# Kernel tuning notes

Measured on AMD Instinct MI355X. Metric: run time of the kernel, lower is better.

Reference implementation:

```python
import jax, jax.numpy as jnp
import numpy as np

N = 100000   # nodes
E = 3200000  # edges
F_IN = 64    # input feature dim
H = 64       # hidden dim
G = 512      # graphs in batch
C = 6        # classes
BN_EPS = 1e-5


def setup_inputs() -> dict:
    key = jax.random.key(0)
    ks = jax.random.split(key, 24)

    def nrm(i, shape, s=0.05):
        return jax.random.normal(ks[i], shape, jnp.float32) * s

    d = {}
    d["x"] = jax.random.normal(ks[0], (N, F_IN), jnp.float32)
    d["edge_index"] = jax.random.randint(ks[1], (2, E), 0, N, dtype=jnp.int32)
    d["batch"] = jnp.sort(jax.random.randint(ks[2], (N,), 0, G, dtype=jnp.int32))
    # GIN MLP weights (conv4 reuses conv3's MLP, matching the original code)
    for li, fin in [(1, F_IN), (2, H), (3, H)]:
        d[f"w{li}a"] = nrm(2 + li * 4, (fin, H))
        d[f"b{li}a"] = jnp.zeros((H,), jnp.float32)
        d[f"w{li}b"] = nrm(3 + li * 4, (H, H))
        d[f"b{li}b"] = jnp.zeros((H,), jnp.float32)
    # learnable eps (train_eps=True, init 0) and BN affine params per layer
    for li in range(1, 5):
        d[f"eps{li}"] = jnp.float32(0.0)
        d[f"g{li}"] = jnp.ones((H,), jnp.float32)
        d[f"be{li}"] = jnp.zeros((H,), jnp.float32)
    d["wfc"] = nrm(20, (2 * H, C))
    d["bfc"] = jnp.zeros((C,), jnp.float32)
    return d


def gin_block(x, src, dst, eps, wa, ba, wb, bb, gamma, beta):
    # neighbor sum aggregation: messages flow src -> dst
    agg = jax.ops.segment_sum(x[src], dst, num_segments=N)
    h = (1.0 + eps) * x + agg
    h = jax.nn.relu(h @ wa + ba) @ wb + bb  # GIN MLP
    h = jax.nn.relu(h)
    # BatchNorm1d over the node dimension (training-mode batch stats)
    mu = h.mean(axis=0)
    var = h.var(axis=0)
    return (h - mu) * jax.lax.rsqrt(var + BN_EPS) * gamma + beta


def reference(x, edge_index, batch,
              w1a, b1a, w1b, b1b, w2a, b2a, w2b, b2b, w3a, b3a, w3b, b3b,
              eps1, g1, be1, eps2, g2, be2, eps3, g3, be3, eps4, g4, be4,
              wfc, bfc):
    src, dst = edge_index[0], edge_index[1]
    h = gin_block(x, src, dst, eps1, w1a, b1a, w1b, b1b, g1, be1)
    h = gin_block(h, src, dst, eps2, w2a, b2a, w2b, b2b, g2, be2)
    h = gin_block(h, src, dst, eps3, w3a, b3a, w3b, b3b, g3, be3)
    # conv4 shares nn3's weights (faithful to the original source)
    h = gin_block(h, src, dst, eps4, w3a, b3a, w3b, b3b, g4, be4)
    cnt = jax.ops.segment_sum(jnp.ones((N, 1), h.dtype), batch, num_segments=G)
    meanp = jax.ops.segment_sum(h, batch, num_segments=G) / jnp.maximum(cnt, 1.0)
    maxp = jax.ops.segment_max(h, batch, num_segments=G)
    maxp = jnp.where(cnt > 0, maxp, 0.0)
    pooled = jnp.concatenate([meanp, maxp], axis=1)  # [G, 128]
    return jax.nn.log_softmax(pooled @ wfc + bfc, axis=1)
```

## Files before the change

### kernel.cpp

```cpp
#include <hip/hip_runtime.h>

#define N_NODES 100000
#define N_EDGES 3200000
#define NGRAPH 512
#define NCLASS 6
#define BN_EPS 1e-5f

#define BSHIFT 8
#define NBUCK 391
#define CHUNK 8192
#define EB 391
#define NBLK_NODE 391
#define FUSG 3125
#define NPART 6250
#define CAST_B 6250
#define BSMAX 12032

typedef unsigned short u16;
typedef unsigned int u32;
typedef __attribute__((ext_vector_type(8))) short bf16x8;
typedef __attribute__((ext_vector_type(4))) float f32x4;
typedef __attribute__((ext_vector_type(2))) float f32x2;

__device__ __forceinline__ float bflo(u32 b) {
    u32 t = b << 16; return __builtin_bit_cast(float, t);
}
__device__ __forceinline__ float bfhi(u32 b) {
    u32 t = b & 0xffff0000u; return __builtin_bit_cast(float, t);
}
__device__ __forceinline__ f32x2 bfpair(u32 b) {
    return (f32x2){bflo(b), bfhi(b)};
}
__device__ __forceinline__ u16 f2bf(float f) {
    u32 u = __builtin_bit_cast(u32, f);
    return (u16)((u + 0x7fffu + ((u >> 16) & 1u)) >> 16);
}

__global__ void k_setup(const float* __restrict__ x, u16* __restrict__ xb,
                        const float* __restrict__ W10, const float* __restrict__ W20,
                        const float* __restrict__ W11, const float* __restrict__ W21,
                        const float* __restrict__ W12, const float* __restrict__ W22,
                        u16* __restrict__ Wtg, float* __restrict__ ss0,
                        const int* __restrict__ dst, const int* __restrict__ batch,
                        int* __restrict__ blockhist, int* __restrict__ gstart,
                        int* __restrict__ rowstart) {
    __shared__ int hist[NBUCK];
    int b = blockIdx.x;
    int t = threadIdx.x;
    if (b < CAST_B) {
        int base = (b * 256 + t) * 4;
        float4 v = *(const float4*)(x + base);
        ushort4 o = make_ushort4(f2bf(v.x), f2bf(v.y), f2bf(v.z), f2bf(v.w));
        *(ushort4*)(xb + base) = o;
    } else if (b < CAST_B + 97) {
        int bb = b - CAST_B;
        if (bb < 96) {
            int e = bb * 256 + t;
            int mat = e >> 12;
            int i = e & 4095;
            const float* s = (mat == 0) ? W10 : (mat == 1) ? W20 : (mat == 2) ? W11
                           : (mat == 3) ? W21 : (mat == 4) ? W12 : W22;
            float v = s[i];
            int k = i >> 6, c = i & 63;
            Wtg[mat * 4608 + c * 72 + k] = f2bf(v);
        } else {
            if (t < 64) ss0[t] = 1.0f;
            else if (t < 128) ss0[t] = 0.0f;
            else if (t == 128) rowstart[N_NODES] = N_EDGES;
        }
    } else if (b < CAST_B + 97 + EB) {
        int be = b - (CAST_B + 97);
        long e0 = (long)be * CHUNK;
        for (int i = t; i < NBUCK; i += 256) hist[i] = 0;
        __syncthreads();
        for (int i = t; i < CHUNK; i += 256) {
            long e = e0 + i;
            if (e < N_EDGES) atomicAdd(&hist[dst[e] >> BSHIFT], 1);
        }
        __syncthreads();
        for (int i = t; i < NBUCK; i += 256) blockhist[be * NBUCK + i] = hist[i];
    } else {
        int i = (b - (CAST_B + 97 + EB)) * 256 + t;
        if (i < N_NODES) {
            int bi = batch[i];
            int bp = (i == 0) ? -1 : batch[i - 1];
            for (int g = bp + 1; g <= bi; ++g) gstart[g] = i;
            if (i == N_NODES - 1)
                for (int g = bi + 1; g <= NGRAPH; ++g) gstart[g] = N_NODES;
        }
    }
}

__global__ void k_scan_cols(int* __restrict__ blockhist, int* __restrict__ colsum) {
    __shared__ int sh[512];
    int k = blockIdx.x;
    int t = threadIdx.x;
    int v = (t < EB) ? blockhist[t * NBUCK + k] : 0;
    sh[t] = v;
    __syncthreads();
    for (int off = 1; off < 512; off <<= 1) {
        int x = (t >= off) ? sh[t - off] : 0;
        __syncthreads();
        sh[t] += x;
        __syncthreads();
    }
    if (t < EB) blockhist[t * NBUCK + k] = sh[t] - v;
    if (t == 511) colsum[k] = sh[511];
}

__global__ __launch_bounds__(512) void k_bscatter(
    const int* __restrict__ src, const int* __restrict__ dst,
    const int* __restrict__ colsum, const int* __restrict__ blockhist,
    int* __restrict__ pairs) {
    __shared__ int sh[512];
    __shared__ int bstart_s[NBUCK];
    __shared__ int cnt[NBUCK];
    __shared__ int cur[NBUCK];
    __shared__ int gbase[NBUCK];
    __shared__ u32 sorted[CHUNK];
    __shared__ u16 kbuf[CHUNK];
    int t = threadIdx.x;
    int b = blockIdx.x;
    long e0 = (long)b * CHUNK;
    int v = (t < NBUCK) ? colsum[t] : 0;
    sh[t] = v;
    if (t < NBUCK) cnt[t] = 0;
    __syncthreads();
    for (int off = 1; off < 512; off <<= 1) {
        int x = (t >= off) ? sh[t - off] : 0;
        __syncthreads();
        sh[t] += x;
        __syncthreads();
    }
    if (t < NBUCK) bstart_s[t] = sh[t] - v;
    __syncthreads();
    for (int i = t; i < CHUNK; i += 512) {
        long e = e0 + i;
        if (e < N_EDGES) atomicAdd(&cnt[dst[e] >> BSHIFT], 1);
    }
    __syncthreads();
    int c = (t < NBUCK) ? cnt[t] : 0;
    sh[t] = c;
    __syncthreads();
    for (int off = 1; off < 512; off <<= 1) {
        int x = (t >= off) ? sh[t - off] : 0;
        __syncthreads();
        sh[t] += x;
        __syncthreads();
    }
    if (t < NBUCK) {
        int excl = sh[t] - c;
        cur[t] = excl;
        gbase[t] = bstart_s[t] + blockhist[b * NBUCK + t] - excl;
    }
    __syncthreads();
    for (int i = t; i < CHUNK; i += 512) {
        long e = e0 + i;
        if (e < N_EDGES) {
            int d = dst[e];
            int k = d >> BSHIFT;
            int r = atomicAdd(&cur[k], 1);
            sorted[r] = ((u32)src[e] << 8) | (u32)(d & 255);
            kbuf[r] = (u16)k;
        }
    }
    __syncthreads();
    int tot = (int)min((long)CHUNK, (long)N_EDGES - e0);
    for (int i = t; i < tot; i += 512)
        pairs[gbase[kbuf[i]] + i] = (int)sorted[i];
}

__global__ __launch_bounds__(512) void k_bsort(
    const int* __restrict__ pairs, const int* __restrict__ colsum,
    int* __restrict__ rowstart, int* __restrict__ esrc) {
    __shared__ int sh[512];
    __shared__ int deg[256];
    __shared__ int cur[256];
    __shared__ u32 ssrc[BSMAX];
    int b = blockIdx.x;
    int t = threadIdx.x;
    int v = (t < NBUCK) ? colsum[t] : 0;
    sh[t] = v;
    if (t < 256) deg[t] = 0;
    __syncthreads();
    for (int off = 1; off < 512; off <<= 1) {
        int x = (t >= off) ? sh[t - off] : 0;
        __syncthreads();
        sh[t] += x;
        __syncthreads();
    }
    int p0 = (b == 0) ? 0 : sh[b - 1];
    int p1 = sh[b];
    int n = p1 - p0;
    __syncthreads();
    for (int i = p0 + t; i < p1; i += 512)
        atomicAdd(&deg[pairs[i] & 255], 1);
    __syncthreads();
    if (t < 256) sh[t] = deg[t];
    __syncthreads();
    for (int off = 1; off < 256; off <<= 1) {
        int x = (t >= off && t < 256) ? sh[t - off] : 0;
        __syncthreads();
        if (t < 256) sh[t] += x;
        __syncthreads();
    }
    if (t < 256) {
        int excl = sh[t] - deg[t];
        cur[t] = excl;
        int node = (b << BSHIFT) + t;
        if (node < N_NODES) rowstart[node] = p0 + excl;
    }
    __syncthreads();
    if (n <= BSMAX) {
        for (int i = p0 + t; i < p1; i += 512) {
            u32 pr = (u32)pairs[i];
            int r = atomicAdd(&cur[pr & 255], 1);
            ssrc[r] = pr >> 8;
        }
        __syncthreads();
        for (int i = t; i < n; i += 512) esrc[p0 + i] = (int)ssrc[i];
    } else {
        for (int i = p0 + t; i < p1; i += 512) {
            u32 pr = (u32)pairs[i];
            int r = atomicAdd(&cur[pr & 255], 1);
            esrc[p0 + r] = (int)(pr >> 8);
        }
    }
}

__global__ void k_bn(const float* __restrict__ partials, const float* __restrict__ g,
                     const float* __restrict__ be, float* __restrict__ ss) {
    __shared__ float sS[256];
    __shared__ float sQ[256];
    int f = blockIdx.x;
    int t = threadIdx.x;
    float aS = 0.f, aQ = 0.f;
    for (int b = t; b < NPART; b += 256) {
        aS += partials[b * 128 + f];
        aQ += partials[b * 128 + 64 + f];
    }
    sS[t] = aS; sQ[t] = aQ;
    __syncthreads();
    for (int off = 128; off >= 1; off >>= 1) {
        if (t < off) { sS[t] += sS[t + off]; sQ[t] += sQ[t + off]; }
        __syncthreads();
    }
    if (t == 0) {
        float mu = sS[0] / (float)N_NODES;
        float var = fmaxf(sQ[0] / (float)N_NODES - mu * mu, 0.f);
        float sc = g[f] * rsqrtf(var + BN_EPS);
        ss[f] = sc;
        ss[64 + f] = be[f] - mu * sc;
    }
}

__global__ __launch_bounds__(128, 5) void k_fused(
    const u16* __restrict__ hin, const float* __restrict__ ss,
    const float* __restrict__ epsp, const int* __restrict__ rowstart,
    const int* __restrict__ esrc, const u16* __restrict__ Wt,
    const float* __restrict__ b1, const float* __restrict__ b2,
    u16* __restrict__ C, float* __restrict__ partials) {
    __shared__ __align__(16) u16 Ain[2][16 * 72];
    __shared__ __align__(16) u16 Hs[2][16 * 72];
    int lane = threadIdx.x & 63;
    int wid = threadIdx.x >> 6;
    int r0 = blockIdx.x * 32 + wid * 16;

    int g = lane >> 3;
    int p = lane & 7;
    int f0 = 8 * p;

    float epsv = 1.0f + epsp[0];
    float4 scA = *(const float4*)(ss + f0);
    float4 scB = *(const float4*)(ss + f0 + 4);
    float4 shA = *(const float4*)(ss + 64 + f0);
    float4 shB = *(const float4*)(ss + 64 + f0 + 4);
    float sc[8] = {scA.x, scA.y, scA.z, scA.w, scB.x, scB.y, scB.z, scB.w};
    float sh[8] = {shA.x, shA.y, shA.z, shA.w, shB.x, shB.y, shB.z, shB.w};

    int rs = rowstart[r0 + ((lane < 17) ? lane : 16)];

    #pragma unroll
    for (int half = 0; half < 2; ++half) {
        int t = g + 8 * half;
        int node = r0 + t;
        int e0 = __shfl(rs, t);
        int e1 = __shfl(rs, t + 1);
        uint4 sb = *(const uint4*)(hin + (unsigned)node * 64u + f0);
        f32x2 aA0 = {0.f, 0.f}, aA1 = {0.f, 0.f}, aA2 = {0.f, 0.f}, aA3 = {0.f, 0.f};
        f32x2 aB0 = {0.f, 0.f}, aB1 = {0.f, 0.f}, aB2 = {0.f, 0.f}, aB3 = {0.f, 0.f};
        int e = e0;
        int e_full = e0 + ((e1 - e0) & ~7);
        for (; e < e_full; e += 8) {
            #pragma unroll
            for (int k = 0; k < 8; ++k) {
                int a = esrc[e + k];
                uint4 v = *(const uint4*)(hin + (unsigned)a * 64u + f0);
                if (k & 1) {
                    aB0 += bfpair(v.x); aB1 += bfpair(v.y);
                    aB2 += bfpair(v.z); aB3 += bfpair(v.w);
                } else {
                    aA0 += bfpair(v.x); aA1 += bfpair(v.y);
                    aA2 += bfpair(v.z); aA3 += bfpair(v.w);
                }
            }
        }
        for (; e < e1; ++e) {
            int a = esrc[e];
            uint4 v = *(const uint4*)(hin + (unsigned)a * 64u + f0);
            aA0 += bfpair(v.x); aA1 += bfpair(v.y);
            aA2 += bfpair(v.z); aA3 += bfpair(v.w);
        }
        f32x2 ac0 = aA0 + aB0, ac1 = aA1 + aB1, ac2 = aA2 + aB2, ac3 = aA3 + aB3;
        float acc[8] = {ac0.x, ac0.y, ac1.x, ac1.y, ac2.x, ac2.y, ac3.x, ac3.y};
        float self[8] = {bflo(sb.x), bfhi(sb.x), bflo(sb.y), bfhi(sb.y),
                         bflo(sb.z), bfhi(sb.z), bflo(sb.w), bfhi(sb.w)};
        float deg = (float)(e1 - e0);
        u32 pk[4];
        #pragma unroll
        for (int k = 0; k < 4; ++k) {
            float oa = sc[2 * k] * (acc[2 * k] + epsv * self[2 * k]) +
                       (deg + epsv) * sh[2 * k];
            float ob = sc[2 * k + 1] * (acc[2 * k + 1] + epsv * self[2 * k + 1]) +
                       (deg + epsv) * sh[2 * k + 1];
            pk[k] = (u32)f2bf(oa) | ((u32)f2bf(ob) << 16);
        }
        u32* arow = (u32*)&Ain[wid][0] + t * 36 + p * 4;
        *(uint4*)arow = make_uint4(pk[0], pk[1], pk[2], pk[3]);
    }

    const u16* Wt2 = Wt + 4608;
    int m = lane & 15;
    int q = lane >> 4;

    bf16x8 a0 = *(const bf16x8*)(&Ain[wid][m * 72 + q * 8]);
    bf16x8 a1 = *(const bf16x8*)(&Ain[wid][m * 72 + 32 + q * 8]);
    f32x4 acc[4];
    #pragma unroll
    for (int c = 0; c < 4; ++c) {
        acc[c] = (f32x4){0.f, 0.f, 0.f, 0.f};
        bf16x8 bA = *(const bf16x8*)(Wt + (c * 16 + m) * 72 + q * 8);
        bf16x8 bB = *(const bf16x8*)(Wt + (c * 16 + m) * 72 + 32 + q * 8);
        acc[c] = __builtin_amdgcn_mfma_f32_16x16x32_bf16(a0, bA, acc[c], 0, 0, 0);
        acc[c] = __builtin_amdgcn_mfma_f32_16x16x32_bf16(a1, bB, acc[c], 0, 0, 0);
    }
    #pragma unroll
    for (int c = 0; c < 4; ++c) {
        int col = c * 16 + m;
        float bb = b1[col];
        #pragma unroll
        for (int r = 0; r < 4; ++r)
            Hs[wid][(q * 4 + r) * 72 + col] = f2bf(fmaxf(acc[c][r] + bb, 0.f));
    }
    bf16x8 h0 = *(const bf16x8*)(&Hs[wid][m * 72 + q * 8]);
    bf16x8 h1 = *(const bf16x8*)(&Hs[wid][m * 72 + 32 + q * 8]);
    f32x4 acc2[4];
    #pragma unroll
    for (int c = 0; c < 4; ++c) {
        acc2[c] = (f32x4){0.f, 0.f, 0.f, 0.f};
        bf16x8 bA = *(const bf16x8*)(Wt2 + (c * 16 + m) * 72 + q * 8);
        bf16x8 bB = *(const bf16x8*)(Wt2 + (c * 16 + m) * 72 + 32 + q * 8);
        acc2[c] = __builtin_amdgcn_mfma_f32_16x16x32_bf16(h0, bA, acc2[c], 0, 0, 0);
        acc2[c] = __builtin_amdgcn_mfma_f32_16x16x32_bf16(h1, bB, acc2[c], 0, 0, 0);
    }
    size_t prow = ((size_t)blockIdx.x * 2 + wid) * 128;
    #pragma unroll
    for (int c = 0; c < 4; ++c) {
        int col = c * 16 + m;
        float bb = b2[col];
        float psum = 0.f, psq = 0.f;
        #pragma unroll
        for (int r = 0; r < 4; ++r) {
            int rg = r0 + q * 4 + r;
            float o = fmaxf(acc2[c][r] + bb, 0.f);
            C[(size_t)rg * 64 + col] = f2bf(o);
            psum += o;
            psq += o * o;
        }
        psum += __shfl_xor(psum, 16);
        psum += __shfl_xor(psum, 32);
        psq += __shfl_xor(psq, 16);
        psq += __shfl_xor(psq, 32);
        if (q == 0) {
            partials[prow + col] = psum;
            partials[prow + 64 + col] = psq;
        }
    }
}

__global__ void k_pool(const u16* __restrict__ h, const float* __restrict__ ss,
                       const int* __restrict__ gstart, const float* __restrict__ wfc,
                       const float* __restrict__ bfc, float* __restrict__ out) {
    __shared__ float smean[2][128];
    __shared__ float smax[2][128];
    __shared__ float lg[2][8];
    int tid = threadIdx.x;
    int lane = tid & 63;
    int w = tid >> 6;
    int gi = w >> 1;
    int part = w & 1;
    int gr = blockIdx.x * 2 + gi;
    int half = lane >> 5;
    int li = lane & 31;
    int f0 = 2 * li;
    float sc0 = ss[f0], sc1 = ss[f0 + 1];
    float sh0 = ss[64 + f0], sh1 = ss[64 + f0 + 1];
    int s0n = gstart[gr], s1n = gstart[gr + 1];
    int cnt = s1n - s0n;
    int mid = s0n + (cnt >> 1);
    int a = part ? mid : s0n;
    int b = part ? s1n : mid;
    float sum0 = 0.f, sum1 = 0.f, mx0 = -3.4e38f, mx1 = -3.4e38f;
    for (int n = a + half; n < b; n += 2) {
        u32 bits = *(const u32*)(h + (size_t)n * 64 + f0);
        float x0 = fmaf(bflo(bits), sc0, sh0);
        float x1 = fmaf(bfhi(bits), sc1, sh1);
        sum0 += x0; sum1 += x1;
        mx0 = fmaxf(mx0, x0); mx1 = fmaxf(mx1, x1);
    }
    sum0 += __shfl_xor(sum0, 32);
    sum1 += __shfl_xor(sum1, 32);
    mx0 = fmaxf(mx0, __shfl_xor(mx0, 32));
    mx1 = fmaxf(mx1, __shfl_xor(mx1, 32));
    if (half == 0 && part == 0) {
        smean[gi][f0] = sum0; smean[gi][f0 + 1] = sum1;
        smax[gi][f0] = mx0;   smax[gi][f0 + 1] = mx1;
    }
    __syncthreads();
    if (half == 0 && part == 1) {
        float m0 = fmaxf(smax[gi][f0], mx0), m1 = fmaxf(smax[gi][f0 + 1], mx1);
        float t0 = smean[gi][f0] + sum0, t1 = smean[gi][f0 + 1] + sum1;
        float fc = fmaxf((float)cnt, 1.f);
        smean[gi][f0] = t0 / fc;
        smean[gi][f0 + 1] = t1 / fc;
        smax[gi][f0] = (cnt > 0) ? m0 : 0.f;
        smax[gi][f0 + 1] = (cnt > 0) ? m1 : 0.f;
    }
    __syncthreads();
    if (part == 0 && lane < NCLASS) {
        float acc = bfc[lane];
        for (int j = 0; j < 64; ++j) acc = fmaf(smean[gi][j], wfc[j * NCLASS + lane], acc);
        for (int j = 0; j < 64; ++j) acc = fmaf(smax[gi][j], wfc[(64 + j) * NCLASS + lane], acc);
        lg[gi][lane] = acc;
    }
    __syncthreads();
    if (part == 0 && lane < NCLASS) {
        float mm = -3.4e38f;
        for (int c = 0; c < NCLASS; ++c) mm = fmaxf(mm, lg[gi][c]);
        float se = 0.f;
        for (int c = 0; c < NCLASS; ++c) se += expf(lg[gi][c] - mm);
        out[gr * NCLASS + lane] = lg[gi][lane] - mm - logf(se);
    }
}


extern "C" void kernel_launch(void* const* d_in, const int* in_sizes, int n_in,
                              void* d_out, int out_size, void* d_ws, size_t ws_size,
                              hipStream_t stream) {
    const float* x = (const float*)d_in[0];
    const int* ei = (const int*)d_in[1];
    const int* batch = (const int*)d_in[2];
    const int* esrc_in = ei;
    const int* edst_in = ei + N_EDGES;

    const float* ba[4] = {(const float*)d_in[4], (const float*)d_in[8],
                          (const float*)d_in[12], (const float*)d_in[12]};
    const float* bb[4] = {(const float*)d_in[6], (const float*)d_in[10],
                          (const float*)d_in[14], (const float*)d_in[14]};
    const float* epsv[4] = {(const float*)d_in[15], (const float*)d_in[18],
                            (const float*)d_in[21], (const float*)d_in[24]};
    const float* gg[4] = {(const float*)d_in[16], (const float*)d_in[19],
                          (const float*)d_in[22], (const float*)d_in[25]};
    const float* bee[4] = {(const float*)d_in[17], (const float*)d_in[20],
                           (const float*)d_in[23], (const float*)d_in[26]};
    const float* wfc = (const float*)d_in[27];
    const float* bfc = (const float*)d_in[28];
    float* out = (float*)d_out;

    char* ws = (char*)d_ws;
    int* pairs = (int*)(ws + 0);
    u16* bufA = (u16*)(ws + 0);
    int* esrc = (int*)(ws + 12800000);
    u16* xb = (u16*)(ws + 25600000);
    u16* bufB = (u16*)(ws + 38400000);
    int* rowstart = (int*)(ws + 51200000);
    int* blockhist = (int*)(ws + 51600128);
    int* colsum = (int*)(ws + 52212480);
    int* gstart = (int*)(ws + 52214528);
    float* partials = (float*)(ws + 52217088);
    float* ssbuf = (float*)(ws + 55417600);
    u16* Wtg = (u16*)(ws + 55420160);

    k_setup<<<CAST_B + 97 + EB + NBLK_NODE, 256, 0, stream>>>(
        x, xb, (const float*)d_in[3], (const float*)d_in[5], (const float*)d_in[7],
        (const float*)d_in[9], (const float*)d_in[11], (const float*)d_in[13],
        Wtg, ssbuf, edst_in, batch, blockhist, gstart, rowstart);
    k_scan_cols<<<NBUCK, 512, 0, stream>>>(blockhist, colsum);
    k_bscatter<<<EB, 512, 0, stream>>>(esrc_in, edst_in, colsum, blockhist, pairs);
    k_bsort<<<NBUCK, 512, 0, stream>>>(pairs, colsum, rowstart, esrc);

    const u16* hb[4] = {xb, bufB, bufA, bufB};
    u16* cb[4] = {bufB, bufA, bufB, bufA};
    for (int L = 0; L < 4; ++L) {
        const u16* wt = Wtg + (size_t)((L < 2) ? L : 2) * 9216;
        k_fused<<<FUSG, 128, 0, stream>>>(hb[L], ssbuf + L * 128, epsv[L], rowstart,
                                          esrc, wt, ba[L], bb[L], cb[L], partials);
        k_bn<<<64, 256, 0, stream>>>(partials, gg[L], bee[L], ssbuf + (L + 1) * 128);
    }

    k_pool<<<NGRAPH / 2, 256, 0, stream>>>(bufA, ssbuf + 4 * 128, gstart, wfc, bfc, out);
}
```

Before: 589.9 us.

## Balance per-wave node degrees and cooperatively prefetch edge indices via shuffles

Each wave ranks its 16 nodes by degree and pairs the heaviest with the lightest (slot g and 15-g), so the 8-lane groups get more even edge counts and divergence within the wave drops. Edge source indices are now loaded cooperatively, one per lane across 8 lanes, and broadcast with shuffles, with the next chunk prefetched so the gather loop no longer waits on a scalar index load. The tail is handled with a masked 8-wide step instead of a scalar loop. This adds shuffle, LDS and ranking overhead, and the masked tail issues dummy loads of row 0.

```diff
diff --git a/kernel.cpp b/kernel.cpp
--- a/kernel.cpp
+++ b/kernel.cpp
@@ -262,12 +262,14 @@
     u16* __restrict__ C, float* __restrict__ partials) {
     __shared__ __align__(16) u16 Ain[2][16 * 72];
     __shared__ __align__(16) u16 Hs[2][16 * 72];
+    __shared__ u16 s_nmap[2][16];
     int lane = threadIdx.x & 63;
     int wid = threadIdx.x >> 6;
     int r0 = blockIdx.x * 32 + wid * 16;
 
     int g = lane >> 3;
     int p = lane & 7;
+    int gb = lane & 56;
     int f0 = 8 * p;
 
     float epsv = 1.0f + epsp[0];
@@ -280,42 +282,74 @@
 
     int rs = rowstart[r0 + ((lane < 17) ? lane : 16)];
 
+    int t16 = lane & 15;
+    int d_self = __shfl(rs, t16 + 1) - __shfl(rs, t16);
+    int rank = 0;
+    {
+        int prev = __shfl(rs, 0);
+        #pragma unroll
+        for (int t = 0; t < 16; ++t) {
+            int nxt = __shfl(rs, t + 1);
+            int dt = nxt - prev; prev = nxt;
+            rank += ((dt > d_self) || (dt == d_self && t < t16)) ? 1 : 0;
+        }
+    }
+    volatile u16* nm = s_nmap[wid];
+    if (lane < 16) nm[rank] = (u16)t16;
+    int ta = nm[g];
+    int tb = nm[15 - g];
+
     #pragma unroll
-    for (int half = 0; half < 2; ++half) {
-        int t = g + 8 * half;
-        int node = r0 + t;
-        int e0 = __shfl(rs, t);
-        int e1 = __shfl(rs, t + 1);
+    for (int el = 0; el < 2; ++el) {
+        int slot = el ? tb : ta;
+        int e0 = __shfl(rs, slot);
+        int e1 = __shfl(rs, slot + 1);
+        int d = e1 - e0;
+        int node = r0 + slot;
         uint4 sb = *(const uint4*)(hin + (unsigned)node * 64u + f0);
         f32x2 aA0 = {0.f, 0.f}, aA1 = {0.f, 0.f}, aA2 = {0.f, 0.f}, aA3 = {0.f, 0.f};
         f32x2 aB0 = {0.f, 0.f}, aB1 = {0.f, 0.f}, aB2 = {0.f, 0.f}, aB3 = {0.f, 0.f};
-        int e = e0;
-        int e_full = e0 + ((e1 - e0) & ~7);
-        for (; e < e_full; e += 8) {
+        if (d > 0) {
+            int idx = esrc[e0 + p];
+            int nfull = (d - 1) >> 3;
+            int rem = d - (nfull << 3);
+            for (int c = 0; c < nfull; ++c) {
+                int nidx = esrc[e0 + (c + 1) * 8 + p];
+                #pragma unroll
+                for (int k = 0; k < 8; ++k) {
+                    int a = __shfl(idx, gb | k);
+                    uint4 v = *(const uint4*)(hin + (unsigned)a * 64u + f0);
+                    if (k & 1) {
+                        aB0 += bfpair(v.x); aB1 += bfpair(v.y);
+                        aB2 += bfpair(v.z); aB3 += bfpair(v.w);
+                    } else {
+                        aA0 += bfpair(v.x); aA1 += bfpair(v.y);
+                        aA2 += bfpair(v.z); aA3 += bfpair(v.w);
+                    }
+                }
+                idx = nidx;
+            }
             #pragma unroll
             for (int k = 0; k < 8; ++k) {
-                int a = esrc[e + k];
+                int a = __shfl(idx, gb | k);
+                a = (k < rem) ? a : 0;
                 uint4 v = *(const uint4*)(hin + (unsigned)a * 64u + f0);
-                if (k & 1) {
-                    aB0 += bfpair(v.x); aB1 += bfpair(v.y);
-                    aB2 += bfpair(v.z); aB3 += bfpair(v.w);
-                } else {
-                    aA0 += bfpair(v.x); aA1 += bfpair(v.y);
-                    aA2 += bfpair(v.z); aA3 += bfpair(v.w);
+                if (k < rem) {
+                    if (k & 1) {
+                        aB0 += bfpair(v.x); aB1 += bfpair(v.y);
+                        aB2 += bfpair(v.z); aB3 += bfpair(v.w);
+                    } else {
+                        aA0 += bfpair(v.x); aA1 += bfpair(v.y);
+                        aA2 += bfpair(v.z); aA3 += bfpair(v.w);
+                    }
                 }
             }
-        }
-        for (; e < e1; ++e) {
-            int a = esrc[e];
-            uint4 v = *(const uint4*)(hin + (unsigned)a * 64u + f0);
-            aA0 += bfpair(v.x); aA1 += bfpair(v.y);
-            aA2 += bfpair(v.z); aA3 += bfpair(v.w);
         }
         f32x2 ac0 = aA0 + aB0, ac1 = aA1 + aB1, ac2 = aA2 + aB2, ac3 = aA3 + aB3;
         float acc[8] = {ac0.x, ac0.y, ac1.x, ac1.y, ac2.x, ac2.y, ac3.x, ac3.y};
         float self[8] = {bflo(sb.x), bfhi(sb.x), bflo(sb.y), bfhi(sb.y),
                          bflo(sb.z), bfhi(sb.z), bflo(sb.w), bfhi(sb.w)};
-        float deg = (float)(e1 - e0);
+        float deg = (float)d;
         u32 pk[4];
         #pragma unroll
         for (int k = 0; k < 4; ++k) {
@@ -325,7 +359,7 @@
                        (deg + epsv) * sh[2 * k + 1];
             pk[k] = (u32)f2bf(oa) | ((u32)f2bf(ob) << 16);
         }
-        u32* arow = (u32*)&Ain[wid][0] + t * 36 + p * 4;
+        u32* arow = (u32*)&Ain[wid][0] + slot * 36 + p * 4;
         *(uint4*)arow = make_uint4(pk[0], pk[1], pk[2], pk[3]);
     }
 
```

Result: faster. 564.1 us (-4.4%).
